# Optimization experiments

Hardware: AMD Instinct MI355X
Metric: run time of the kernel (lower is better)

The kernel has to match this reference:

```python
import jax, jax.numpy as jnp
import numpy as np

B, N, CA, CS, CZ, H, NQ, NK = 2, 16384, 128, 128, 16, 4, 32, 128
DH = CA // H
NB = N // NQ


def _ln(x, gamma=None, eps=1e-5):
    m = jnp.mean(x, -1, keepdims=True)
    v = jnp.var(x, -1, keepdims=True)
    y = (x - m) * jax.lax.rsqrt(v + eps)
    return y if gamma is None else y * gamma


def _adaln(a, s, gamma_s, Wg, bg, Wskip):
    # AF3 Algorithm 26: LN(a) without affine; LN(s) with scale, no offset;
    # out = sigmoid(Linear(s)) * a + LinearNoBias(s)
    a_n = _ln(a)
    s_n = _ln(s, gamma_s)
    return jax.nn.sigmoid(s_n @ Wg + bg) * a_n + s_n @ Wskip


def setup_inputs():
    key = jax.random.key(0)
    ks = jax.random.split(key, 20)
    def nrm(i, shape, scale=0.02):
        return jax.random.normal(ks[i], shape, jnp.float32) * scale
    return {
        "a": jax.random.normal(ks[0], (B, N, CA), jnp.float32),
        "s": jax.random.normal(ks[1], (B, N, CS), jnp.float32),
        "z": jax.random.normal(ks[2], (B, NB, NQ, NK, CZ), jnp.float32),
        "apb_gamma_s": jnp.ones((CS,), jnp.float32),
        "apb_Wg": nrm(3, (CS, CA)),
        "apb_bg": jnp.zeros((CA,), jnp.float32),
        "apb_Wskip": nrm(4, (CS, CA)),
        "Wq": nrm(5, (CA, CA)), "bq": jnp.zeros((CA,), jnp.float32),
        "Wk": nrm(6, (CA, CA)), "Wv": nrm(7, (CA, CA)),
        "Wgate": nrm(8, (CA, CA)), "Wo": nrm(9, (CA, CA)),
        "gamma_z": jnp.ones((CZ,), jnp.float32),
        "Wz": nrm(10, (CZ, H)),
        "Ws_last": nrm(11, (CS, CA)),
        "bs_last": jnp.full((CA,), -2.0, jnp.float32),
        "ct_gamma_s": jnp.ones((CS,), jnp.float32),
        "ct_Wg": nrm(12, (CS, CA)), "ct_bg": jnp.zeros((CA,), jnp.float32),
        "ct_Wskip": nrm(13, (CS, CA)),
        "Wa1": nrm(14, (CA, 2 * CA)), "Wa2": nrm(15, (CA, 2 * CA)),
        "Wb": nrm(16, (2 * CA, CA)),
        "Ws": nrm(17, (CS, CA)), "bs": jnp.full((CA,), -2.0, jnp.float32),
        "n_queries": NQ, "n_keys": NK,
    }


def reference(a, s, z, apb_gamma_s, apb_Wg, apb_bg, apb_Wskip, Wq, bq, Wk, Wv,
              Wgate, Wo, gamma_z, Wz, Ws_last, bs_last, ct_gamma_s, ct_Wg,
              ct_bg, ct_Wskip, Wa1, Wa2, Wb, Ws, bs, n_queries, n_keys):
    nq, nk = int(n_queries), int(n_keys)
    nb = N // nq
    # ---- AttentionPairBias, local windowed attention ----
    a1 = _adaln(a, s, apb_gamma_s, apb_Wg, apb_bg, apb_Wskip)  # [B,N,CA]
    # trunked pair bias: [B,nb,nq,nk,H] -> [B,H,nb,nq,nk]
    bias = jnp.transpose(_ln(z, gamma_z) @ Wz, (0, 4, 1, 2, 3))
    q = (a1 @ Wq + bq).reshape(B, N, H, DH).transpose(0, 2, 1, 3)
    k = (a1 @ Wk).reshape(B, N, H, DH).transpose(0, 2, 1, 3)
    v = (a1 @ Wv).reshape(B, N, H, DH).transpose(0, 2, 1, 3)
    qb = q.reshape(B, H, nb, nq, DH)
    pad = (nk - nq) // 2
    # centered key window per query block
    idx = (jnp.arange(nb) * nq - pad)[:, None] + jnp.arange(nk)[None, :]  # [nb,nk]
    valid = (idx >= 0) & (idx < N)
    idxc = jnp.clip(idx, 0, N - 1)
    kb = k[:, :, idxc]  # [B,H,nb,nk,DH]
    vb = v[:, :, idxc]
    scores = jnp.einsum('bhnqd,bhnkd->bhnqk', qb, kb) / np.sqrt(DH).astype(np.float32) + bias
    scores = jnp.where(valid[None, None, :, None, :], scores, -1e9)
    attn = jax.nn.softmax(scores, axis=-1)
    o = jnp.einsum('bhnqk,bhnkd->bhnqd', attn, vb)  # [B,H,nb,nq,DH]
    o = o.reshape(B, H, N, DH).transpose(0, 2, 1, 3).reshape(B, N, CA)
    g = jax.nn.sigmoid(a1 @ Wgate)  # per-channel gating
    attn_out = (g * o) @ Wo
    b_out = jax.nn.sigmoid(s @ Ws_last + bs_last) * attn_out
    # ---- ConditionedTransitionBlock (Alg 25) ----
    a3 = _adaln(a, s, ct_gamma_s, ct_Wg, ct_bg, ct_Wskip)
    t = jax.nn.silu(a3 @ Wa1) * (a3 @ Wa2)
    ct_out = jax.nn.sigmoid(s @ Ws + bs) * (t @ Wb)
    # Alg 23: a = b + ConditionedTransitionBlock(a, s)
    return b_out + ct_out
```

## Files before the change

### kernel.cpp

```cpp
#include <hip/hip_runtime.h>

typedef _Float16 f16;
typedef f16 f16x8 __attribute__((ext_vector_type(8)));
typedef f16 f16x4 __attribute__((ext_vector_type(4)));
typedef f16 f16x2 __attribute__((ext_vector_type(2)));
typedef float f32x4 __attribute__((ext_vector_type(4)));

#define MFMA16(a,b,c) __builtin_amdgcn_mfma_f32_16x16x32_f16((a),(b),(c),0,0,0)

static __device__ __forceinline__ f16x8 ld8(const f16* p){ return *(const f16x8*)p; }
static __device__ __forceinline__ float sigm(float x){ return 1.f/(1.f + __expf(-x)); }

__global__ __launch_bounds__(256) void k_prep(
    const float* __restrict__ apb_gamma, const float* __restrict__ apb_Wg, const float* __restrict__ apb_Wskip,
    const float* __restrict__ ct_gamma,  const float* __restrict__ ct_Wg,  const float* __restrict__ ct_Wskip,
    const float* __restrict__ Wq, const float* __restrict__ Wk, const float* __restrict__ Wv, const float* __restrict__ Wgate,
    const float* __restrict__ Wsl, const float* __restrict__ Wss,
    const float* __restrict__ Wa1, const float* __restrict__ Wa2,
    const float* __restrict__ Wo, const float* __restrict__ Wb,
    const float* __restrict__ gamma_z, const float* __restrict__ Wz,
    f16* __restrict__ wA, f16* __restrict__ wC, f16* __restrict__ wQK, f16* __restrict__ wVG,
    f16* __restrict__ wSG, f16* __restrict__ wAB, f16* __restrict__ wO, f16* __restrict__ wBt,
    float* __restrict__ wzg)
{
  const int t0 = blockIdx.x*256 + threadIdx.x;
  const int stride = gridDim.x*256;
  for (int i = t0; i < 256*128; i += stride){
    const int n = i >> 7, k = i & 127;
    const int m = n & 127;
    wA[i]  = (f16)(((n<128) ? apb_Wg[k*128+m] : apb_Wskip[k*128+m]) * apb_gamma[k]);
    wC[i]  = (f16)(((n<128) ? ct_Wg[k*128+m]  : ct_Wskip[k*128+m])  * ct_gamma[k]);
    wQK[i] = (f16)((n<128) ? Wq[k*128+m] : Wk[k*128+m]);
    wVG[i] = (f16)((n<128) ? Wv[k*128+m] : Wgate[k*128+m]);
    wSG[i] = (f16)((n<128) ? Wsl[k*128+m] : Wss[k*128+m]);
  }
  for (int i = t0; i < 512*128; i += stride){
    const int n = i >> 7, k = i & 127;
    wAB[i] = (f16)((n & 1) ? Wa2[k*256 + (n>>1)] : Wa1[k*256 + (n>>1)]);
  }
  for (int i = t0; i < 128*128; i += stride){
    const int n = i >> 7, k = i & 127;
    wO[i] = (f16)Wo[k*128+n];
  }
  for (int i = t0; i < 128*256; i += stride){
    const int n = i >> 8, k = i & 255;
    wBt[i] = (f16)Wb[k*128+n];
  }
  if (t0 < 64) wzg[t0] = gamma_z[t0 & 15] * Wz[(t0 & 15)*4 + (t0 >> 4)];
}

__global__ __launch_bounds__(256) void k_ln(const float* __restrict__ A, const float* __restrict__ S,
    f16* __restrict__ An, f16* __restrict__ Sn, f16* __restrict__ Sh)
{
  const int w = threadIdx.x >> 6, l = threadIdx.x & 63;
  const size_t row = (size_t)blockIdx.x*4 + w;
  const float2 av = *(const float2*)(A + row*128 + l*2);
  const float2 sv = *(const float2*)(S + row*128 + l*2);
  float sa = av.x + av.y, qa = av.x*av.x + av.y*av.y;
  float ss = sv.x + sv.y, qs = sv.x*sv.x + sv.y*sv.y;
  #pragma unroll
  for (int o = 32; o; o >>= 1){
    sa += __shfl_xor(sa, o); qa += __shfl_xor(qa, o);
    ss += __shfl_xor(ss, o); qs += __shfl_xor(qs, o);
  }
  const float ma = sa*(1.f/128.f), va = qa*(1.f/128.f) - ma*ma;
  const float ms = ss*(1.f/128.f), vs = qs*(1.f/128.f) - ms*ms;
  const float ra = rsqrtf(va + 1e-5f), rs = rsqrtf(vs + 1e-5f);
  f16x2 o1; o1[0] = (f16)((av.x-ma)*ra); o1[1] = (f16)((av.y-ma)*ra);
  *(f16x2*)(An + row*128 + l*2) = o1;
  f16x2 o2; o2[0] = (f16)((sv.x-ms)*rs); o2[1] = (f16)((sv.y-ms)*rs);
  *(f16x2*)(Sn + row*128 + l*2) = o2;
  f16x2 o3; o3[0] = (f16)sv.x; o3[1] = (f16)sv.y;
  *(f16x2*)(Sh + row*128 + l*2) = o3;
}

__global__ __launch_bounds__(256) void k_adaln(
    const f16* __restrict__ Sn, const f16* __restrict__ An,
    const f16* __restrict__ wA, const f16* __restrict__ wC,
    const float* __restrict__ bgA, const float* __restrict__ bgC,
    f16* __restrict__ A1, f16* __restrict__ A3)
{
  const int l = threadIdx.x & 63, w = threadIdx.x >> 6;
  const int c = l & 15, q4 = l >> 4;
  const int n0 = blockIdx.y * 16;
  f16x8 bA0[4], bA1[4], bC0[4], bC1[4];
  #pragma unroll
  for (int kc = 0; kc < 4; kc++){
    bA0[kc] = ld8(wA + (size_t)(n0 + c)*128 + kc*32 + q4*8);
    bA1[kc] = ld8(wA + (size_t)(128 + n0 + c)*128 + kc*32 + q4*8);
    bC0[kc] = ld8(wC + (size_t)(n0 + c)*128 + kc*32 + q4*8);
    bC1[kc] = ld8(wC + (size_t)(128 + n0 + c)*128 + kc*32 + q4*8);
  }
  const float bvA = bgA[n0 + c], bvC = bgC[n0 + c];
  for (int mi = 0; mi < 4; mi++){
    const int mbase = blockIdx.x*256 + w*64 + mi*16;
    const f16* xp = Sn + (size_t)(mbase + c)*128 + q4*8;
    f32x4 dA0 = {0,0,0,0}, dA1 = {0,0,0,0}, dC0 = {0,0,0,0}, dC1 = {0,0,0,0};
    #pragma unroll
    for (int kc = 0; kc < 4; kc++){
      f16x8 av = ld8(xp + kc*32);
      dA0 = MFMA16(av, bA0[kc], dA0);
      dA1 = MFMA16(av, bA1[kc], dA1);
      dC0 = MFMA16(av, bC0[kc], dC0);
      dC1 = MFMA16(av, bC1[kc], dC1);
    }
    #pragma unroll
    for (int r = 0; r < 4; r++){
      const size_t row = mbase + q4*4 + r;
      const float anv = (float)An[row*128 + n0 + c];
      A1[row*128 + n0 + c] = (f16)(sigm(dA0[r] + bvA)*anv + dA1[r]);
      A3[row*128 + n0 + c] = (f16)(sigm(dC0[r] + bvC)*anv + dC1[r]);
    }
  }
}

__global__ __launch_bounds__(256) void k_gates(
    const f16* __restrict__ X, const f16* __restrict__ Wt,
    const float* __restrict__ bias0, const float* __restrict__ bias1,
    f16* __restrict__ out0, f16* __restrict__ out1)
{
  const int l = threadIdx.x & 63, w = threadIdx.x >> 6;
  const int c = l & 15, q4 = l >> 4;
  const int n0 = blockIdx.y * 16;
  f16x8 b0[4], b1[4];
  #pragma unroll
  for (int kc = 0; kc < 4; kc++){
    b0[kc] = ld8(Wt + (size_t)(n0 + c)*128 + kc*32 + q4*8);
    b1[kc] = ld8(Wt + (size_t)(128 + n0 + c)*128 + kc*32 + q4*8);
  }
  const float bv0 = bias0[n0 + c], bv1 = bias1[n0 + c];
  for (int mi = 0; mi < 4; mi++){
    const int mbase = blockIdx.x*256 + w*64 + mi*16;
    const f16* xp = X + (size_t)(mbase + c)*128 + q4*8;
    f32x4 d0 = {0,0,0,0}, d1 = {0,0,0,0};
    #pragma unroll
    for (int kc = 0; kc < 4; kc++){
      f16x8 av = ld8(xp + kc*32);
      d0 = MFMA16(av, b0[kc], d0);
      d1 = MFMA16(av, b1[kc], d1);
    }
    #pragma unroll
    for (int r = 0; r < 4; r++){
      const size_t row = mbase + q4*4 + r;
      out0[row*128 + n0 + c] = (f16)sigm(d0[r] + bv0);
      out1[row*128 + n0 + c] = (f16)sigm(d1[r] + bv1);
    }
  }
}

__global__ __launch_bounds__(256) void k_qkvg(
    const f16* __restrict__ X, const f16* __restrict__ wQK, const f16* __restrict__ wVG,
    const float* __restrict__ bq,
    f16* __restrict__ Qo, f16* __restrict__ Ko, f16* __restrict__ Vt, f16* __restrict__ Go)
{
  const int l = threadIdx.x & 63, w = threadIdx.x >> 6;
  const int c = l & 15, q4 = l >> 4;
  const int n0 = blockIdx.y * 16;
  f16x8 bQ[4], bK[4], bV[4], bG[4];
  #pragma unroll
  for (int kc = 0; kc < 4; kc++){
    bQ[kc] = ld8(wQK + (size_t)(n0 + c)*128 + kc*32 + q4*8);
    bK[kc] = ld8(wQK + (size_t)(128 + n0 + c)*128 + kc*32 + q4*8);
    bV[kc] = ld8(wVG + (size_t)(n0 + c)*128 + kc*32 + q4*8);
    bG[kc] = ld8(wVG + (size_t)(128 + n0 + c)*128 + kc*32 + q4*8);
  }
  const float bvq = bq[n0 + c];
  for (int mi = 0; mi < 4; mi++){
    const int mbase = blockIdx.x*256 + w*64 + mi*16;
    const f16* xp = X + (size_t)(mbase + c)*128 + q4*8;
    f32x4 dQ = {0,0,0,0}, dK = {0,0,0,0}, dV = {0,0,0,0}, dG = {0,0,0,0};
    #pragma unroll
    for (int kc = 0; kc < 4; kc++){
      f16x8 av = ld8(xp + kc*32);
      dQ = MFMA16(av, bQ[kc], dQ);
      dK = MFMA16(av, bK[kc], dK);
      dV = MFMA16(av, bV[kc], dV);
      dG = MFMA16(av, bG[kc], dG);
    }
    #pragma unroll
    for (int r = 0; r < 4; r++){
      const size_t row = mbase + q4*4 + r;
      Qo[row*128 + n0 + c] = (f16)((dQ[r] + bvq)*0.17677669529663687f);
      Ko[row*128 + n0 + c] = (f16)dK[r];
      Go[row*128 + n0 + c] = (f16)sigm(dG[r]);
    }
    f16x4 vv;
    #pragma unroll
    for (int r = 0; r < 4; r++) vv[r] = (f16)dV[r];
    const int bidx = mbase >> 14;
    const int ntk  = (mbase & 16383) + q4*4;
    *(f16x4*)(Vt + ((size_t)bidx*128 + n0 + c)*16384 + ntk) = vv;
  }
}

__global__ __launch_bounds__(256) void k_ab(const f16* __restrict__ X, const f16* __restrict__ Wt,
                                            f16* __restrict__ T)
{
  const int l = threadIdx.x & 63, w = threadIdx.x >> 6;
  const int c = l & 15, q4 = l >> 4;
  const int n0 = blockIdx.y * 32;
  f16x8 b0[4], b1[4];
  #pragma unroll
  for (int kc = 0; kc < 4; kc++){
    b0[kc] = ld8(Wt + (size_t)(n0 + c)*128 + kc*32 + q4*8);
    b1[kc] = ld8(Wt + (size_t)(n0 + 16 + c)*128 + kc*32 + q4*8);
  }
  for (int mi = 0; mi < 4; mi++){
    const int mbase = blockIdx.x*256 + w*64 + mi*16;
    const f16* xp = X + (size_t)(mbase + c)*128 + q4*8;
    f32x4 d0 = {0,0,0,0}, d1 = {0,0,0,0};
    #pragma unroll
    for (int kc = 0; kc < 4; kc++){
      f16x8 av = ld8(xp + kc*32);
      d0 = MFMA16(av, b0[kc], d0);
      d1 = MFMA16(av, b1[kc], d1);
    }
    #pragma unroll
    for (int tile = 0; tile < 2; tile++){
      #pragma unroll
      for (int r = 0; r < 4; r++){
        const float dv = tile ? d1[r] : d0[r];
        const float ov = __shfl_xor(dv, 1);
        const float u  = (c & 1) ? ov : dv;
        const float vv = (c & 1) ? dv : ov;
        const float tvv = (u * sigm(u)) * vv;
        if (!(c & 1)){
          const size_t row = mbase + q4*4 + r;
          T[row*256 + ((n0 + tile*16 + c) >> 1)] = (f16)tvv;
        }
      }
    }
  }
}

__global__ __launch_bounds__(512) void k_attn(const f16* __restrict__ Q, const f16* __restrict__ K,
    const f16* __restrict__ VT, const float* __restrict__ Z, const float* __restrict__ WZG,
    f16* __restrict__ Og)
{
  __shared__ f16 upb[17408];
  __shared__ float wzg_s[64];
  const int tid = threadIdx.x;
  const int b = blockIdx.x >> 9, nb = blockIdx.x & 511;
  if (tid < 64) wzg_s[tid] = WZG[tid];
  __syncthreads();
  #pragma unroll
  for (int i = 0; i < 8; i++){
    const int p  = tid + i*512;
    const int qq = p >> 7, kk = p & 127;
    const float* zp = Z + ((((size_t)b*512 + nb)*32 + qq)*128 + kk)*16;
    const float4 z0 = *(const float4*)(zp);
    const float4 z1 = *(const float4*)(zp + 4);
    const float4 z2 = *(const float4*)(zp + 8);
    const float4 z3 = *(const float4*)(zp + 12);
    const float xs[16] = {z0.x,z0.y,z0.z,z0.w, z1.x,z1.y,z1.z,z1.w,
                          z2.x,z2.y,z2.z,z2.w, z3.x,z3.y,z3.z,z3.w};
    float sm = 0.f, sq = 0.f;
    #pragma unroll
    for (int cc = 0; cc < 16; cc++){ sm += xs[cc]; sq += xs[cc]*xs[cc]; }
    const float mean = sm*(1.f/16.f);
    const float var  = sq*(1.f/16.f) - mean*mean;
    const float rs   = rsqrtf(var + 1e-5f);
    #pragma unroll
    for (int h = 0; h < 4; h++){
      float acc = 0.f;
      #pragma unroll
      for (int cc = 0; cc < 16; cc++) acc += (xs[cc]-mean)*wzg_s[h*16+cc];
      upb[(h*32 + qq)*132 + kk] = (f16)(acc*rs);
    }
  }
  __syncthreads();

  const int l = tid & 63, w = tid >> 6;
  const int c = l & 15, q4 = l >> 4;
  const int h = w >> 1, qh = w & 1, m0 = qh*16;
  const f16x8 aq = ld8(Q + ((size_t)b*16384 + (size_t)nb*32 + m0 + c)*128 + h*32 + q4*8);
  const long kbase = (long)b*16384 + (long)nb*32 - 48;
  f32x4 sc[8];
  #pragma unroll
  for (int nt = 0; nt < 8; nt++){
    const f16x8 bf = ld8(K + (kbase + nt*16 + c)*128 + h*32 + q4*8);
    f32x4 zz = {0.f,0.f,0.f,0.f};
    sc[nt] = MFMA16(aq, bf, zz);
  }
  #pragma unroll
  for (int nt = 0; nt < 8; nt++){
    const int key = nt*16 + c;
    const long kt = (long)nb*32 - 48 + key;
    const bool inv = (kt < 0) || (kt >= 16384);
    #pragma unroll
    for (int r = 0; r < 4; r++){
      const float v = sc[nt][r] + (float)upb[(h*32 + m0 + q4*4 + r)*132 + key];
      sc[nt][r] = inv ? -1e9f : v;
    }
  }
  #pragma unroll
  for (int r = 0; r < 4; r++){
    float mx = sc[0][r];
    #pragma unroll
    for (int nt = 1; nt < 8; nt++) mx = fmaxf(mx, sc[nt][r]);
    #pragma unroll
    for (int o = 8; o; o >>= 1) mx = fmaxf(mx, __shfl_xor(mx, o));
    float sum = 0.f;
    #pragma unroll
    for (int nt = 0; nt < 8; nt++){ const float e = __expf(sc[nt][r]-mx); sc[nt][r] = e; sum += e; }
    #pragma unroll
    for (int o = 8; o; o >>= 1) sum += __shfl_xor(sum, o);
    const float inv = 1.f/sum;
    #pragma unroll
    for (int nt = 0; nt < 8; nt++) sc[nt][r] *= inv;
  }
  __syncthreads();
  #pragma unroll
  for (int nt = 0; nt < 8; nt++)
    #pragma unroll
    for (int r = 0; r < 4; r++)
      upb[(w*16 + q4*4 + r)*136 + nt*16 + c] = (f16)sc[nt][r];
  const f16* vb = VT + ((long)b*128)*16384 + (long)nb*32 - 48;
  f32x4 o0 = {0.f,0.f,0.f,0.f}, o1 = {0.f,0.f,0.f,0.f};
  #pragma unroll
  for (int kc = 0; kc < 4; kc++){
    const f16x8 pa = *(const f16x8*)&upb[(w*16 + c)*136 + kc*32 + q4*8];
    const f16x8 v0 = ld8(vb + (long)(h*32 + c)*16384 + kc*32 + q4*8);
    const f16x8 v1 = ld8(vb + (long)(h*32 + 16 + c)*16384 + kc*32 + q4*8);
    o0 = MFMA16(pa, v0, o0);
    o1 = MFMA16(pa, v1, o1);
  }
  #pragma unroll
  for (int r = 0; r < 4; r++){
    const size_t tok = (size_t)b*16384 + (size_t)nb*32 + m0 + q4*4 + r;
    Og[tok*128 + h*32 + c]      = (f16)o0[r];
    Og[tok*128 + h*32 + 16 + c] = (f16)o1[r];
  }
}

__global__ __launch_bounds__(256) void k_final(const f16* __restrict__ G, const f16* __restrict__ O,
    const f16* __restrict__ T, const f16* __restrict__ Wot, const f16* __restrict__ Wbt,
    const f16* __restrict__ GL, const f16* __restrict__ GS, float* __restrict__ out)
{
  const int l = threadIdx.x & 63, w = threadIdx.x >> 6;
  const int c = l & 15, q4 = l >> 4;
  #pragma unroll
  for (int nt = 0; nt < 2; nt++){
    const int cb = blockIdx.y*32 + nt*16;
    f16x8 bo[4], bb[8];
    #pragma unroll
    for (int kc = 0; kc < 4; kc++) bo[kc] = ld8(Wot + (size_t)(cb + c)*128 + kc*32 + q4*8);
    #pragma unroll
    for (int kc = 0; kc < 8; kc++) bb[kc] = ld8(Wbt + (size_t)(cb + c)*256 + kc*32 + q4*8);
    for (int mi = 0; mi < 4; mi++){
      const int mbase = blockIdx.x*256 + w*64 + mi*16;
      f32x4 d1 = {0.f,0.f,0.f,0.f}, d2 = {0.f,0.f,0.f,0.f};
      const f16* gp = G + (size_t)(mbase + c)*128 + q4*8;
      const f16* op = O + (size_t)(mbase + c)*128 + q4*8;
      #pragma unroll
      for (int kc = 0; kc < 4; kc++){
        const f16x8 av = ld8(gp + kc*32) * ld8(op + kc*32);
        d1 = MFMA16(av, bo[kc], d1);
      }
      const f16* tp = T + (size_t)(mbase + c)*256 + q4*8;
      #pragma unroll
      for (int kc = 0; kc < 8; kc++) d2 = MFMA16(ld8(tp + kc*32), bb[kc], d2);
      #pragma unroll
      for (int r = 0; r < 4; r++){
        const size_t row = mbase + q4*4 + r;
        const float glv = (float)GL[row*128 + cb + c];
        const float gsv = (float)GS[row*128 + cb + c];
        out[row*128 + cb + c] = glv*d1[r] + gsv*d2[r];
      }
    }
  }
}

extern "C" void kernel_launch(void* const* d_in, const int* in_sizes, int n_in,
                              void* d_out, int out_size, void* d_ws, size_t ws_size,
                              hipStream_t stream)
{
  (void)in_sizes; (void)n_in; (void)out_size; (void)ws_size;
  const float* a        = (const float*)d_in[0];
  const float* s        = (const float*)d_in[1];
  const float* z        = (const float*)d_in[2];
  const float* apb_gamma= (const float*)d_in[3];
  const float* apb_Wg   = (const float*)d_in[4];
  const float* apb_bg   = (const float*)d_in[5];
  const float* apb_Wskip= (const float*)d_in[6];
  const float* Wq       = (const float*)d_in[7];
  const float* bq       = (const float*)d_in[8];
  const float* Wk       = (const float*)d_in[9];
  const float* Wv       = (const float*)d_in[10];
  const float* Wgate    = (const float*)d_in[11];
  const float* Wo       = (const float*)d_in[12];
  const float* gamma_z  = (const float*)d_in[13];
  const float* Wz       = (const float*)d_in[14];
  const float* Wsl      = (const float*)d_in[15];
  const float* bsl      = (const float*)d_in[16];
  const float* ct_gamma = (const float*)d_in[17];
  const float* ct_Wg    = (const float*)d_in[18];
  const float* ct_bg    = (const float*)d_in[19];
  const float* ct_Wskip = (const float*)d_in[20];
  const float* Wa1      = (const float*)d_in[21];
  const float* Wa2      = (const float*)d_in[22];
  const float* Wb       = (const float*)d_in[23];
  const float* Wss      = (const float*)d_in[24];
  const float* bss      = (const float*)d_in[25];

  f16* W0 = (f16*)d_ws;
  const size_t SL = (size_t)32768*128;
  f16* an = W0 + 0*SL;   f16* qv = an;
  f16* sn = W0 + 1*SL;   f16* kv = sn;
  f16* sh = W0 + 2*SL;   f16* vt = sh;
  f16* a1 = W0 + 3*SL;   f16* ov = a1;
  f16* a3 = W0 + 4*SL;
  f16* gl = W0 + 5*SL;
  f16* gs = W0 + 6*SL;
  f16* gv = W0 + 7*SL;
  f16* tv = W0 + 8*SL;
  f16* wA  = W0 + 10*SL;
  f16* wC  = wA  + 256*128;
  f16* wQK = wC  + 256*128;
  f16* wVG = wQK + 256*128;
  f16* wSG = wVG + 256*128;
  f16* wAB = wSG + 256*128;
  f16* wO  = wAB + 512*128;
  f16* wBt = wO  + 128*128;
  float* wzg = (float*)(wBt + 128*256);

  k_prep<<<dim3(64),256,0,stream>>>(apb_gamma,apb_Wg,apb_Wskip, ct_gamma,ct_Wg,ct_Wskip,
      Wq,Wk,Wv,Wgate, Wsl,Wss, Wa1,Wa2, Wo,Wb, gamma_z,Wz,
      wA,wC,wQK,wVG,wSG,wAB,wO,wBt,wzg);
  k_ln<<<dim3(8192),256,0,stream>>>(a,s,an,sn,sh);
  k_adaln<<<dim3(128,8),256,0,stream>>>(sn,an,wA,wC,apb_bg,ct_bg,a1,a3);
  k_gates<<<dim3(128,8),256,0,stream>>>(sh,wSG,bsl,bss,gl,gs);
  k_qkvg<<<dim3(128,8),256,0,stream>>>(a1,wQK,wVG,bq,qv,kv,vt,gv);
  k_ab<<<dim3(128,16),256,0,stream>>>(a3,wAB,tv);
  k_attn<<<dim3(1024),512,0,stream>>>(qv,kv,vt,z,wzg,ov);
  k_final<<<dim3(128,4),256,0,stream>>>(gv,ov,tv,wO,wBt,gl,gs,(float*)d_out);
}
```

Before: 602.4 us.

## Fuse layernorm, adaLN, QKVG, transition and gate projections into one kernel

```diff
diff --git a/kernel.cpp b/kernel.cpp
--- a/kernel.cpp
+++ b/kernel.cpp
@@ -21,7 +21,7 @@
     const float* __restrict__ gamma_z, const float* __restrict__ Wz,
     f16* __restrict__ wA, f16* __restrict__ wC, f16* __restrict__ wQK, f16* __restrict__ wVG,
     f16* __restrict__ wSG, f16* __restrict__ wAB, f16* __restrict__ wO, f16* __restrict__ wBt,
-    float* __restrict__ wzg)
+    float* __restrict__ wzg, float* __restrict__ Slv, float* __restrict__ Ssv)
 {
   const int t0 = blockIdx.x*256 + threadIdx.x;
   const int stride = gridDim.x*256;
@@ -36,7 +36,7 @@
   }
   for (int i = t0; i < 512*128; i += stride){
     const int n = i >> 7, k = i & 127;
-    wAB[i] = (f16)((n & 1) ? Wa2[k*256 + (n>>1)] : Wa1[k*256 + (n>>1)]);
+    wAB[i] = (f16)((n < 256) ? Wa1[k*256 + n] : Wa2[k*256 + (n-256)]);
   }
   for (int i = t0; i < 128*128; i += stride){
     const int n = i >> 7, k = i & 127;
@@ -47,187 +47,210 @@
     wBt[i] = (f16)Wb[k*128+n];
   }
   if (t0 < 64) wzg[t0] = gamma_z[t0 & 15] * Wz[(t0 & 15)*4 + (t0 >> 4)];
+  if (t0 < 256){
+    const int cc = t0 & 127;
+    const float* Wp = (t0 >= 128) ? Wss : Wsl;
+    float acc = 0.f;
+    for (int k = 0; k < 128; k++) acc += Wp[k*128 + cc];
+    if (t0 >= 128) Ssv[cc] = acc; else Slv[cc] = acc;
+  }
 }
 
-__global__ __launch_bounds__(256) void k_ln(const float* __restrict__ A, const float* __restrict__ S,
-    f16* __restrict__ An, f16* __restrict__ Sn, f16* __restrict__ Sh)
+__global__ __launch_bounds__(256) void k_pre(
+    const float* __restrict__ A, const float* __restrict__ S,
+    const f16* __restrict__ wA, const f16* __restrict__ wC,
+    const f16* __restrict__ wQK, const f16* __restrict__ wVG,
+    const f16* __restrict__ wSG, const f16* __restrict__ wAB,
+    const float* __restrict__ bgA, const float* __restrict__ bgC,
+    const float* __restrict__ bq, const float* __restrict__ bsl, const float* __restrict__ bss,
+    const float* __restrict__ Slv, const float* __restrict__ Ssv,
+    f16* __restrict__ Qo, f16* __restrict__ Ko, f16* __restrict__ Vt, f16* __restrict__ Go,
+    f16* __restrict__ T, f16* __restrict__ GL, f16* __restrict__ GS)
 {
-  const int w = threadIdx.x >> 6, l = threadIdx.x & 63;
-  const size_t row = (size_t)blockIdx.x*4 + w;
-  const float2 av = *(const float2*)(A + row*128 + l*2);
-  const float2 sv = *(const float2*)(S + row*128 + l*2);
-  float sa = av.x + av.y, qa = av.x*av.x + av.y*av.y;
-  float ss = sv.x + sv.y, qs = sv.x*sv.x + sv.y*sv.y;
-  #pragma unroll
-  for (int o = 32; o; o >>= 1){
-    sa += __shfl_xor(sa, o); qa += __shfl_xor(qa, o);
-    ss += __shfl_xor(ss, o); qs += __shfl_xor(qs, o);
-  }
-  const float ma = sa*(1.f/128.f), va = qa*(1.f/128.f) - ma*ma;
-  const float ms = ss*(1.f/128.f), vs = qs*(1.f/128.f) - ms*ms;
-  const float ra = rsqrtf(va + 1e-5f), rs = rsqrtf(vs + 1e-5f);
-  f16x2 o1; o1[0] = (f16)((av.x-ma)*ra); o1[1] = (f16)((av.y-ma)*ra);
-  *(f16x2*)(An + row*128 + l*2) = o1;
-  f16x2 o2; o2[0] = (f16)((sv.x-ms)*rs); o2[1] = (f16)((sv.y-ms)*rs);
-  *(f16x2*)(Sn + row*128 + l*2) = o2;
-  f16x2 o3; o3[0] = (f16)sv.x; o3[1] = (f16)sv.y;
-  *(f16x2*)(Sh + row*128 + l*2) = o3;
-}
-
-__global__ __launch_bounds__(256) void k_adaln(
-    const f16* __restrict__ Sn, const f16* __restrict__ An,
-    const f16* __restrict__ wA, const f16* __restrict__ wC,
-    const float* __restrict__ bgA, const float* __restrict__ bgC,
-    f16* __restrict__ A1, f16* __restrict__ A3)
-{
-  const int l = threadIdx.x & 63, w = threadIdx.x >> 6;
+  __shared__ f16 lsn[64*136];
+  __shared__ f16 lan[64*136];
+  __shared__ f16 la1[64*136];
+  __shared__ f16 la3[64*136];
+  __shared__ float lsm[64], lsd[64];
+  const int tid = threadIdx.x;
+  const size_t rbase = (size_t)blockIdx.x * 64;
+
+  {
+    const int row = tid >> 2, part = tid & 3;
+    const size_t gr = rbase + row;
+    {
+      const float* sp = S + gr*128 + part*32;
+      float v[32];
+      #pragma unroll
+      for (int j = 0; j < 8; j++){
+        const float4 t4 = ((const float4*)sp)[j];
+        v[j*4+0]=t4.x; v[j*4+1]=t4.y; v[j*4+2]=t4.z; v[j*4+3]=t4.w;
+      }
+      float sm = 0.f, sq = 0.f;
+      #pragma unroll
+      for (int j = 0; j < 32; j++){ sm += v[j]; sq += v[j]*v[j]; }
+      sm += __shfl_xor(sm,1); sq += __shfl_xor(sq,1);
+      sm += __shfl_xor(sm,2); sq += __shfl_xor(sq,2);
+      const float mean = sm*(1.f/128.f);
+      const float var  = sq*(1.f/128.f) - mean*mean;
+      const float rstd = rsqrtf(var + 1e-5f);
+      if (part == 0){ lsm[row] = mean; lsd[row] = (var + 1e-5f)*rstd; }
+      #pragma unroll
+      for (int j = 0; j < 4; j++){
+        f16x8 o;
+        #pragma unroll
+        for (int e = 0; e < 8; e++) o[e] = (f16)((v[j*8+e]-mean)*rstd);
+        *(f16x8*)&lsn[row*136 + part*32 + j*8] = o;
+      }
+    }
+    {
+      const float* ap = A + gr*128 + part*32;
+      float v[32];
+      #pragma unroll
+      for (int j = 0; j < 8; j++){
+        const float4 t4 = ((const float4*)ap)[j];
+        v[j*4+0]=t4.x; v[j*4+1]=t4.y; v[j*4+2]=t4.z; v[j*4+3]=t4.w;
+      }
+      float sm = 0.f, sq = 0.f;
+      #pragma unroll
+      for (int j = 0; j < 32; j++){ sm += v[j]; sq += v[j]*v[j]; }
+      sm += __shfl_xor(sm,1); sq += __shfl_xor(sq,1);
+      sm += __shfl_xor(sm,2); sq += __shfl_xor(sq,2);
+      const float mean = sm*(1.f/128.f);
+      const float var  = sq*(1.f/128.f) - mean*mean;
+      const float rstd = rsqrtf(var + 1e-5f);
+      #pragma unroll
+      for (int j = 0; j < 4; j++){
+        f16x8 o;
+        #pragma unroll
+        for (int e = 0; e < 8; e++) o[e] = (f16)((v[j*8+e]-mean)*rstd);
+        *(f16x8*)&lan[row*136 + part*32 + j*8] = o;
+      }
+    }
+  }
+  __syncthreads();
+
+  const int l = tid & 63, w = tid >> 6;
   const int c = l & 15, q4 = l >> 4;
-  const int n0 = blockIdx.y * 16;
-  f16x8 bA0[4], bA1[4], bC0[4], bC1[4];
-  #pragma unroll
-  for (int kc = 0; kc < 4; kc++){
-    bA0[kc] = ld8(wA + (size_t)(n0 + c)*128 + kc*32 + q4*8);
-    bA1[kc] = ld8(wA + (size_t)(128 + n0 + c)*128 + kc*32 + q4*8);
-    bC0[kc] = ld8(wC + (size_t)(n0 + c)*128 + kc*32 + q4*8);
-    bC1[kc] = ld8(wC + (size_t)(128 + n0 + c)*128 + kc*32 + q4*8);
-  }
-  const float bvA = bgA[n0 + c], bvC = bgC[n0 + c];
-  for (int mi = 0; mi < 4; mi++){
-    const int mbase = blockIdx.x*256 + w*64 + mi*16;
-    const f16* xp = Sn + (size_t)(mbase + c)*128 + q4*8;
-    f32x4 dA0 = {0,0,0,0}, dA1 = {0,0,0,0}, dC0 = {0,0,0,0}, dC1 = {0,0,0,0};
+
+  for (int jj = 0; jj < 4; jj++){
+    const int job = jj*4 + w;
+    const int n0 = (job >> 1)*16;
+    const int mat = job & 1;
+    const f16* W = mat ? wC : wA;
+    f16* dst = mat ? la3 : la1;
+    const float bv = (mat ? bgC : bgA)[n0 + c];
+    f16x8 b0[4], b1[4];
     #pragma unroll
     for (int kc = 0; kc < 4; kc++){
-      f16x8 av = ld8(xp + kc*32);
-      dA0 = MFMA16(av, bA0[kc], dA0);
-      dA1 = MFMA16(av, bA1[kc], dA1);
-      dC0 = MFMA16(av, bC0[kc], dC0);
-      dC1 = MFMA16(av, bC1[kc], dC1);
-    }
-    #pragma unroll
-    for (int r = 0; r < 4; r++){
-      const size_t row = mbase + q4*4 + r;
-      const float anv = (float)An[row*128 + n0 + c];
-      A1[row*128 + n0 + c] = (f16)(sigm(dA0[r] + bvA)*anv + dA1[r]);
-      A3[row*128 + n0 + c] = (f16)(sigm(dC0[r] + bvC)*anv + dC1[r]);
-    }
-  }
-}
-
-__global__ __launch_bounds__(256) void k_gates(
-    const f16* __restrict__ X, const f16* __restrict__ Wt,
-    const float* __restrict__ bias0, const float* __restrict__ bias1,
-    f16* __restrict__ out0, f16* __restrict__ out1)
-{
-  const int l = threadIdx.x & 63, w = threadIdx.x >> 6;
-  const int c = l & 15, q4 = l >> 4;
-  const int n0 = blockIdx.y * 16;
-  f16x8 b0[4], b1[4];
-  #pragma unroll
-  for (int kc = 0; kc < 4; kc++){
-    b0[kc] = ld8(Wt + (size_t)(n0 + c)*128 + kc*32 + q4*8);
-    b1[kc] = ld8(Wt + (size_t)(128 + n0 + c)*128 + kc*32 + q4*8);
-  }
-  const float bv0 = bias0[n0 + c], bv1 = bias1[n0 + c];
-  for (int mi = 0; mi < 4; mi++){
-    const int mbase = blockIdx.x*256 + w*64 + mi*16;
-    const f16* xp = X + (size_t)(mbase + c)*128 + q4*8;
-    f32x4 d0 = {0,0,0,0}, d1 = {0,0,0,0};
+      b0[kc] = ld8(W + (size_t)(n0 + c)*128 + kc*32 + q4*8);
+      b1[kc] = ld8(W + (size_t)(128 + n0 + c)*128 + kc*32 + q4*8);
+    }
+    for (int mi = 0; mi < 4; mi++){
+      f32x4 d0 = {0,0,0,0}, d1 = {0,0,0,0};
+      #pragma unroll
+      for (int kc = 0; kc < 4; kc++){
+        const f16x8 av = *(const f16x8*)&lsn[(mi*16 + c)*136 + kc*32 + q4*8];
+        d0 = MFMA16(av, b0[kc], d0);
+        d1 = MFMA16(av, b1[kc], d1);
+      }
+      #pragma unroll
+      for (int r = 0; r < 4; r++){
+        const int row = mi*16 + q4*4 + r;
+        const float anv = (float)lan[row*136 + n0 + c];
+        dst[row*136 + n0 + c] = (f16)(sigm(d0[r] + bv)*anv + d1[r]);
+      }
+    }
+  }
+  __syncthreads();
+
+  for (int jj = 0; jj < 2; jj++){
+    const int n0 = (jj*4 + w)*16;
+    f16x8 bQ[4], bK[4], bV[4], bG[4];
     #pragma unroll
     for (int kc = 0; kc < 4; kc++){
-      f16x8 av = ld8(xp + kc*32);
-      d0 = MFMA16(av, b0[kc], d0);
-      d1 = MFMA16(av, b1[kc], d1);
-    }
-    #pragma unroll
-    for (int r = 0; r < 4; r++){
-      const size_t row = mbase + q4*4 + r;
-      out0[row*128 + n0 + c] = (f16)sigm(d0[r] + bv0);
-      out1[row*128 + n0 + c] = (f16)sigm(d1[r] + bv1);
-    }
-  }
-}
-
-__global__ __launch_bounds__(256) void k_qkvg(
-    const f16* __restrict__ X, const f16* __restrict__ wQK, const f16* __restrict__ wVG,
-    const float* __restrict__ bq,
-    f16* __restrict__ Qo, f16* __restrict__ Ko, f16* __restrict__ Vt, f16* __restrict__ Go)
-{
-  const int l = threadIdx.x & 63, w = threadIdx.x >> 6;
-  const int c = l & 15, q4 = l >> 4;
-  const int n0 = blockIdx.y * 16;
-  f16x8 bQ[4], bK[4], bV[4], bG[4];
-  #pragma unroll
-  for (int kc = 0; kc < 4; kc++){
-    bQ[kc] = ld8(wQK + (size_t)(n0 + c)*128 + kc*32 + q4*8);
-    bK[kc] = ld8(wQK + (size_t)(128 + n0 + c)*128 + kc*32 + q4*8);
-    bV[kc] = ld8(wVG + (size_t)(n0 + c)*128 + kc*32 + q4*8);
-    bG[kc] = ld8(wVG + (size_t)(128 + n0 + c)*128 + kc*32 + q4*8);
-  }
-  const float bvq = bq[n0 + c];
-  for (int mi = 0; mi < 4; mi++){
-    const int mbase = blockIdx.x*256 + w*64 + mi*16;
-    const f16* xp = X + (size_t)(mbase + c)*128 + q4*8;
-    f32x4 dQ = {0,0,0,0}, dK = {0,0,0,0}, dV = {0,0,0,0}, dG = {0,0,0,0};
+      bQ[kc] = ld8(wQK + (size_t)(n0 + c)*128 + kc*32 + q4*8);
+      bK[kc] = ld8(wQK + (size_t)(128 + n0 + c)*128 + kc*32 + q4*8);
+      bV[kc] = ld8(wVG + (size_t)(n0 + c)*128 + kc*32 + q4*8);
+      bG[kc] = ld8(wVG + (size_t)(128 + n0 + c)*128 + kc*32 + q4*8);
+    }
+    const float bvq = bq[n0 + c];
+    for (int mi = 0; mi < 4; mi++){
+      f32x4 dQ = {0,0,0,0}, dK = {0,0,0,0}, dV = {0,0,0,0}, dG = {0,0,0,0};
+      #pragma unroll
+      for (int kc = 0; kc < 4; kc++){
+        const f16x8 av = *(const f16x8*)&la1[(mi*16 + c)*136 + kc*32 + q4*8];
+        dQ = MFMA16(av, bQ[kc], dQ);
+        dK = MFMA16(av, bK[kc], dK);
+        dV = MFMA16(av, bV[kc], dV);
+        dG = MFMA16(av, bG[kc], dG);
+      }
+      #pragma unroll
+      for (int r = 0; r < 4; r++){
+        const size_t grow = rbase + mi*16 + q4*4 + r;
+        Qo[grow*128 + n0 + c] = (f16)((dQ[r] + bvq)*0.17677669529663687f);
+        Ko[grow*128 + n0 + c] = (f16)dK[r];
+        Go[grow*128 + n0 + c] = (f16)sigm(dG[r]);
+      }
+      f16x4 vv;
+      #pragma unroll
+      for (int r = 0; r < 4; r++) vv[r] = (f16)dV[r];
+      const int bidx = (int)(rbase >> 14);
+      const int ntk  = (int)(rbase & 16383) + mi*16 + q4*4;
+      *(f16x4*)(Vt + ((size_t)bidx*128 + n0 + c)*16384 + ntk) = vv;
+    }
+  }
+
+  for (int jj = 0; jj < 4; jj++){
+    const int n0t = (jj*4 + w)*16;
+    f16x8 b1v[4], b2v[4];
     #pragma unroll
     for (int kc = 0; kc < 4; kc++){
-      f16x8 av = ld8(xp + kc*32);
-      dQ = MFMA16(av, bQ[kc], dQ);
-      dK = MFMA16(av, bK[kc], dK);
-      dV = MFMA16(av, bV[kc], dV);
-      dG = MFMA16(av, bG[kc], dG);
-    }
-    #pragma unroll
-    for (int r = 0; r < 4; r++){
-      const size_t row = mbase + q4*4 + r;
-      Qo[row*128 + n0 + c] = (f16)((dQ[r] + bvq)*0.17677669529663687f);
-      Ko[row*128 + n0 + c] = (f16)dK[r];
-      Go[row*128 + n0 + c] = (f16)sigm(dG[r]);
-    }
-    f16x4 vv;
-    #pragma unroll
-    for (int r = 0; r < 4; r++) vv[r] = (f16)dV[r];
-    const int bidx = mbase >> 14;
-    const int ntk  = (mbase & 16383) + q4*4;
-    *(f16x4*)(Vt + ((size_t)bidx*128 + n0 + c)*16384 + ntk) = vv;
-  }
-}
-
-__global__ __launch_bounds__(256) void k_ab(const f16* __restrict__ X, const f16* __restrict__ Wt,
-                                            f16* __restrict__ T)
-{
-  const int l = threadIdx.x & 63, w = threadIdx.x >> 6;
-  const int c = l & 15, q4 = l >> 4;
-  const int n0 = blockIdx.y * 32;
-  f16x8 b0[4], b1[4];
-  #pragma unroll
-  for (int kc = 0; kc < 4; kc++){
-    b0[kc] = ld8(Wt + (size_t)(n0 + c)*128 + kc*32 + q4*8);
-    b1[kc] = ld8(Wt + (size_t)(n0 + 16 + c)*128 + kc*32 + q4*8);
-  }
-  for (int mi = 0; mi < 4; mi++){
-    const int mbase = blockIdx.x*256 + w*64 + mi*16;
-    const f16* xp = X + (size_t)(mbase + c)*128 + q4*8;
-    f32x4 d0 = {0,0,0,0}, d1 = {0,0,0,0};
+      b1v[kc] = ld8(wAB + (size_t)(n0t + c)*128 + kc*32 + q4*8);
+      b2v[kc] = ld8(wAB + (size_t)(256 + n0t + c)*128 + kc*32 + q4*8);
+    }
+    for (int mi = 0; mi < 4; mi++){
+      f32x4 d0 = {0,0,0,0}, d1 = {0,0,0,0};
+      #pragma unroll
+      for (int kc = 0; kc < 4; kc++){
+        const f16x8 av = *(const f16x8*)&la3[(mi*16 + c)*136 + kc*32 + q4*8];
+        d0 = MFMA16(av, b1v[kc], d0);
+        d1 = MFMA16(av, b2v[kc], d1);
+      }
+      #pragma unroll
+      for (int r = 0; r < 4; r++){
+        const size_t grow = rbase + mi*16 + q4*4 + r;
+        const float u = d0[r];
+        T[grow*256 + n0t + c] = (f16)((u*sigm(u))*d1[r]);
+      }
+    }
+  }
+
+  for (int jj = 0; jj < 2; jj++){
+    const int n0 = (jj*4 + w)*16;
+    f16x8 b0[4], b1[4];
     #pragma unroll
     for (int kc = 0; kc < 4; kc++){
-      f16x8 av = ld8(xp + kc*32);
-      d0 = MFMA16(av, b0[kc], d0);
-      d1 = MFMA16(av, b1[kc], d1);
-    }
-    #pragma unroll
-    for (int tile = 0; tile < 2; tile++){
+      b0[kc] = ld8(wSG + (size_t)(n0 + c)*128 + kc*32 + q4*8);
+      b1[kc] = ld8(wSG + (size_t)(128 + n0 + c)*128 + kc*32 + q4*8);
+    }
+    const float slc = Slv[n0 + c], ssc = Ssv[n0 + c];
+    const float bl = bsl[n0 + c],  bs2 = bss[n0 + c];
+    for (int mi = 0; mi < 4; mi++){
+      f32x4 d0 = {0,0,0,0}, d1 = {0,0,0,0};
+      #pragma unroll
+      for (int kc = 0; kc < 4; kc++){
+        const f16x8 av = *(const f16x8*)&lsn[(mi*16 + c)*136 + kc*32 + q4*8];
+        d0 = MFMA16(av, b0[kc], d0);
+        d1 = MFMA16(av, b1[kc], d1);
+      }
       #pragma unroll
       for (int r = 0; r < 4; r++){
-        const float dv = tile ? d1[r] : d0[r];
-        const float ov = __shfl_xor(dv, 1);
-        const float u  = (c & 1) ? ov : dv;
-        const float vv = (c & 1) ? dv : ov;
-        const float tvv = (u * sigm(u)) * vv;
-        if (!(c & 1)){
-          const size_t row = mbase + q4*4 + r;
-          T[row*256 + ((n0 + tile*16 + c) >> 1)] = (f16)tvv;
-        }
+        const int row = mi*16 + q4*4 + r;
+        const size_t grow = rbase + row;
+        const float mn = lsm[row], sd = lsd[row];
+        GL[grow*128 + n0 + c] = (f16)sigm(d0[r]*sd + mn*slc + bl);
+        GS[grow*128 + n0 + c] = (f16)sigm(d1[r]*sd + mn*ssc + bs2);
       }
     }
   }
@@ -339,34 +362,30 @@
 {
   const int l = threadIdx.x & 63, w = threadIdx.x >> 6;
   const int c = l & 15, q4 = l >> 4;
-  #pragma unroll
-  for (int nt = 0; nt < 2; nt++){
-    const int cb = blockIdx.y*32 + nt*16;
-    f16x8 bo[4], bb[8];
-    #pragma unroll
-    for (int kc = 0; kc < 4; kc++) bo[kc] = ld8(Wot + (size_t)(cb + c)*128 + kc*32 + q4*8);
-    #pragma unroll
-    for (int kc = 0; kc < 8; kc++) bb[kc] = ld8(Wbt + (size_t)(cb + c)*256 + kc*32 + q4*8);
-    for (int mi = 0; mi < 4; mi++){
-      const int mbase = blockIdx.x*256 + w*64 + mi*16;
-      f32x4 d1 = {0.f,0.f,0.f,0.f}, d2 = {0.f,0.f,0.f,0.f};
-      const f16* gp = G + (size_t)(mbase + c)*128 + q4*8;
-      const f16* op = O + (size_t)(mbase + c)*128 + q4*8;
-      #pragma unroll
-      for (int kc = 0; kc < 4; kc++){
-        const f16x8 av = ld8(gp + kc*32) * ld8(op + kc*32);
-        d1 = MFMA16(av, bo[kc], d1);
-      }
-      const f16* tp = T + (size_t)(mbase + c)*256 + q4*8;
-      #pragma unroll
-      for (int kc = 0; kc < 8; kc++) d2 = MFMA16(ld8(tp + kc*32), bb[kc], d2);
-      #pragma unroll
-      for (int r = 0; r < 4; r++){
-        const size_t row = mbase + q4*4 + r;
-        const float glv = (float)GL[row*128 + cb + c];
-        const float gsv = (float)GS[row*128 + cb + c];
-        out[row*128 + cb + c] = glv*d1[r] + gsv*d2[r];
-      }
+  const int mbase = blockIdx.x*64 + w*16;
+  f16x8 ag[4], at[8];
+  const f16* gp = G + (size_t)(mbase + c)*128 + q4*8;
+  const f16* op = O + (size_t)(mbase + c)*128 + q4*8;
+  #pragma unroll
+  for (int kc = 0; kc < 4; kc++) ag[kc] = ld8(gp + kc*32) * ld8(op + kc*32);
+  const f16* tp = T + (size_t)(mbase + c)*256 + q4*8;
+  #pragma unroll
+  for (int kc = 0; kc < 8; kc++) at[kc] = ld8(tp + kc*32);
+  for (int nt = 0; nt < 8; nt++){
+    const int cb = nt*16;
+    f32x4 d1 = {0,0,0,0}, d2 = {0,0,0,0};
+    #pragma unroll
+    for (int kc = 0; kc < 4; kc++)
+      d1 = MFMA16(ag[kc], ld8(Wot + (size_t)(cb + c)*128 + kc*32 + q4*8), d1);
+    #pragma unroll
+    for (int kc = 0; kc < 8; kc++)
+      d2 = MFMA16(at[kc], ld8(Wbt + (size_t)(cb + c)*256 + kc*32 + q4*8), d2);
+    #pragma unroll
+    for (int r = 0; r < 4; r++){
+      const size_t row = mbase + q4*4 + r;
+      const float glv = (float)GL[row*128 + cb + c];
+      const float gsv = (float)GS[row*128 + cb + c];
+      out[row*128 + cb + c] = glv*d1[r] + gsv*d2[r];
     }
   }
 }
@@ -405,16 +424,15 @@
 
   f16* W0 = (f16*)d_ws;
   const size_t SL = (size_t)32768*128;
-  f16* an = W0 + 0*SL;   f16* qv = an;
-  f16* sn = W0 + 1*SL;   f16* kv = sn;
-  f16* sh = W0 + 2*SL;   f16* vt = sh;
-  f16* a1 = W0 + 3*SL;   f16* ov = a1;
-  f16* a3 = W0 + 4*SL;
-  f16* gl = W0 + 5*SL;
-  f16* gs = W0 + 6*SL;
-  f16* gv = W0 + 7*SL;
-  f16* tv = W0 + 8*SL;
-  f16* wA  = W0 + 10*SL;
+  f16* qv = W0 + 0*SL;
+  f16* kv = W0 + 1*SL;
+  f16* vt = W0 + 2*SL;
+  f16* gv = W0 + 3*SL;
+  f16* tv = W0 + 4*SL;
+  f16* gl = W0 + 6*SL;
+  f16* gs = W0 + 7*SL;
+  f16* ov = W0 + 8*SL;
+  f16* wA  = W0 + 9*SL;
   f16* wC  = wA  + 256*128;
   f16* wQK = wC  + 256*128;
   f16* wVG = wQK + 256*128;
@@ -423,15 +441,14 @@
   f16* wO  = wAB + 512*128;
   f16* wBt = wO  + 128*128;
   float* wzg = (float*)(wBt + 128*256);
+  float* Slv = wzg + 64;
+  float* Ssv = Slv + 128;
 
   k_prep<<<dim3(64),256,0,stream>>>(apb_gamma,apb_Wg,apb_Wskip, ct_gamma,ct_Wg,ct_Wskip,
       Wq,Wk,Wv,Wgate, Wsl,Wss, Wa1,Wa2, Wo,Wb, gamma_z,Wz,
-      wA,wC,wQK,wVG,wSG,wAB,wO,wBt,wzg);
-  k_ln<<<dim3(8192),256,0,stream>>>(a,s,an,sn,sh);
-  k_adaln<<<dim3(128,8),256,0,stream>>>(sn,an,wA,wC,apb_bg,ct_bg,a1,a3);
-  k_gates<<<dim3(128,8),256,0,stream>>>(sh,wSG,bsl,bss,gl,gs);
-  k_qkvg<<<dim3(128,8),256,0,stream>>>(a1,wQK,wVG,bq,qv,kv,vt,gv);
-  k_ab<<<dim3(128,16),256,0,stream>>>(a3,wAB,tv);
+      wA,wC,wQK,wVG,wSG,wAB,wO,wBt,wzg,Slv,Ssv);
+  k_pre<<<dim3(512),256,0,stream>>>(a,s, wA,wC,wQK,wVG,wSG,wAB,
+      apb_bg,ct_bg,bq,bsl,bss,Slv,Ssv, qv,kv,vt,gv,tv,gl,gs);
   k_attn<<<dim3(1024),512,0,stream>>>(qv,kv,vt,z,wzg,ov);
-  k_final<<<dim3(128,4),256,0,stream>>>(gv,ov,tv,wO,wBt,gl,gs,(float*)d_out);
+  k_final<<<dim3(512),256,0,stream>>>(gv,ov,tv,wO,wBt,gl,gs,(float*)d_out);
 }
```

After: 534.9 us. 1.13x faster.
